# Performance work log

Hardware: AMD Instinct MI355X
Metric: run time of the kernel (lower is better)

## Reference

```python
import jax, jax.numpy as jnp
import numpy as np

SHARED_DIM = 512
ENC_IN = 512
LATENT = 16
BATCH = 65536
NUM_CLASSES = 16


def setup_inputs() -> dict:
    key = jax.random.key(0)
    ks = jax.random.split(key, 12)
    s = 1.0 / np.sqrt(SHARED_DIM)
    si = 1.0 / np.sqrt(ENC_IN)
    return {
        "x": jax.random.normal(ks[0], (BATCH, ENC_IN), dtype=jnp.float32),
        # shared MLP: two ReLU hiddens + identity output (rlkit Mlp)
        "W0": jax.random.uniform(ks[1], (SHARED_DIM, ENC_IN), jnp.float32, -si, si),
        "b0": jnp.zeros((SHARED_DIM,), jnp.float32),
        "W1": jax.random.uniform(ks[2], (SHARED_DIM, SHARED_DIM), jnp.float32, -s, s),
        "b1": jnp.zeros((SHARED_DIM,), jnp.float32),
        "W2": jax.random.uniform(ks[3], (SHARED_DIM, SHARED_DIM), jnp.float32, -s, s),
        "b2": jnp.zeros((SHARED_DIM,), jnp.float32),
        # class encoder (router)
        "Wc": jax.random.uniform(ks[4], (NUM_CLASSES, SHARED_DIM), jnp.float32, -s, s),
        "bc": jnp.zeros((NUM_CLASSES,), jnp.float32),
        # per-class gaussian experts, stacked: [K, 2*latent, shared_dim]
        "Wg": jax.random.uniform(ks[5], (NUM_CLASSES, 2 * LATENT, SHARED_DIM), jnp.float32, -s, s),
        "bg": jnp.zeros((NUM_CLASSES, 2 * LATENT), jnp.float32),
    }


def reference(x, W0, b0, W1, b1, W2, b2, Wc, bc, Wg, bg):
    # shared encoder: ReLU MLP with identity output layer
    m = jax.nn.relu(x @ W0.T + b0)
    m = jax.nn.relu(m @ W1.T + b1)
    m = m @ W2.T + b2                      # [B, D]
    # router: softmax over classes, then most-likely class per sample
    y_probs = jax.nn.softmax(m @ Wc.T + bc, axis=-1)   # [B, K]
    y = jnp.argmax(y_probs, axis=1)                    # [B]
    # evaluate ALL per-class experts densely (as the original does)
    mu_sigma = jnp.einsum('bd,ked->bke', m, Wg) + bg   # [B, K, 2L]
    mu = mu_sigma[..., :LATENT]                        # Normal mean; sampler='mean'
    # gather the selected class's mean per sample
    z = jnp.take_along_axis(mu, y[:, None, None], axis=1)[:, 0, :]  # [B, L]
    return (z, y)
```

## Files before the change

kernel.cpp:

```cpp
#include <hip/hip_runtime.h>
#include <hip/hip_bf16.h>

typedef __attribute__((ext_vector_type(8))) short short8;
typedef __attribute__((ext_vector_type(16))) float floatx16;
typedef __attribute__((ext_vector_type(4))) float floatx4;

#define AS1 __attribute__((address_space(1)))
#define AS3 __attribute__((address_space(3)))

constexpr int MM = 65536;
constexpr int KK = 512;
constexpr int NN = 512;

#define GM 128
#define GN 128
#define GK 32
#define LDT 40

__device__ __forceinline__ unsigned short bf16_rn(float v) {
  unsigned u = __float_as_uint(v);
  return (unsigned short)((u + 0x7FFFu + ((u >> 16) & 1u)) >> 16);
}
__device__ __forceinline__ float bf16_to_f32(unsigned short h) {
  return __uint_as_float((unsigned)h << 16);
}

__global__ __launch_bounds__(256) void split_kernel(
    const float* __restrict__ src, unsigned short* __restrict__ h,
    unsigned short* __restrict__ l, int n4) {
  int i = blockIdx.x * 256 + threadIdx.x;
  if (i >= n4) return;
  float4 v = ((const float4*)src)[i];
  ushort4 hv, lv;
  hv.x = bf16_rn(v.x); lv.x = bf16_rn(v.x - bf16_to_f32(hv.x));
  hv.y = bf16_rn(v.y); lv.y = bf16_rn(v.y - bf16_to_f32(hv.y));
  hv.z = bf16_rn(v.z); lv.z = bf16_rn(v.z - bf16_to_f32(hv.z));
  hv.w = bf16_rn(v.w); lv.w = bf16_rn(v.w - bf16_to_f32(hv.w));
  ((ushort4*)h)[i] = hv;
  ((ushort4*)l)[i] = lv;
}

template<bool RELU>
__global__ __launch_bounds__(512, 1) void gemm_mfma(
    const unsigned short* __restrict__ Ah, const unsigned short* __restrict__ Al,
    const unsigned short* __restrict__ Wh, const unsigned short* __restrict__ Wl,
    const float* __restrict__ bias,
    unsigned short* __restrict__ Ch, unsigned short* __restrict__ Cl) {
  __shared__ __align__(16) unsigned short smem[65536];
  const int tid = threadIdx.x;
  const int lane = tid & 63;
  const int wid = tid >> 6;
  const int wr = wid >> 2;
  const int wc = wid & 3;
  const int nwg = gridDim.x;
  const int hw  = blockIdx.x;
  const int logical = (hw & 7) * (nwg >> 3) + (hw >> 3);
  const int bm = logical >> 1, bn = logical & 1;
  const size_t Abase = (size_t)bm * 256 * KK;
  const size_t Bbase = (size_t)bn * 256 * KK;

  const int sarr  = wid >> 1;
  const int rbase = (wid & 1) * 128;
  const unsigned short* gsrc = (sarr == 0) ? Ah : (sarr == 1) ? Al
                             : (sarr == 2) ? Wh : Wl;
  const size_t tb = (sarr < 2) ? Abase : Bbase;
  const int rowl = lane >> 2;
  const int gch  = (lane & 3) ^ ((lane >> 3) & 3);
  const unsigned short* gbase = gsrc + tb + (size_t)(rbase + rowl) * KK + gch * 8;
  unsigned short* ldst = smem + sarr * 8192 + rbase * 32;

  auto stage2 = [&](int buf, int kk, int p) {
#pragma unroll
    for (int j = p * 2; j < p * 2 + 2; ++j) {
      __builtin_amdgcn_global_load_lds(
          (const AS1 unsigned int*)(gbase + (size_t)(j * 16) * KK + kk),
          (AS3 unsigned int*)(ldst + buf * 32768 + j * 16 * 32),
          16, 0, 0);
    }
  };

  floatx16 acc[4][2];
#pragma unroll
  for (int i = 0; i < 4; ++i)
#pragma unroll
    for (int j = 0; j < 2; ++j)
#pragma unroll
      for (int r = 0; r < 16; ++r) acc[i][j][r] = 0.f;

#pragma unroll
  for (int p = 0; p < 4; ++p) stage2(0, 0, p);

  const int swz = (lane >> 1) & 3;
#pragma unroll
  for (int t = 0; t < 16; ++t) {
    const int cur = t & 1;
    const unsigned short* base = smem + cur * 32768;
    short8 fbh[2], fbl[2];
#pragma unroll
    for (int p = 0; p < 4; ++p) {
      const int ks = p >> 1, h = p & 1;
      const int ch = ks * 2 + (lane >> 5);
      const int sw = (ch ^ swz) * 8;
      short8 fah[2], fal[2];

      if (p == 0) {
        if (t < 15) {
          stage2(cur ^ 1, (t + 1) * GK, 0);
          asm volatile("s_waitcnt vmcnt(2)" ::: "memory");
        } else {
          asm volatile("s_waitcnt vmcnt(0)" ::: "memory");
        }
        __builtin_amdgcn_s_barrier();
        __builtin_amdgcn_sched_barrier(0);
      }

#pragma unroll
      for (int q = 0; q < 2; ++q) {
        int row = wr * 128 + (h * 2 + q) * 32 + (lane & 31);
        fah[q] = *(const short8*)(base + row * 32 + sw);
        fal[q] = *(const short8*)(base + 8192 + row * 32 + sw);
      }
      if (h == 0) {
#pragma unroll
        for (int si = 0; si < 2; ++si) {
          int col = wc * 64 + si * 32 + (lane & 31);
          fbh[si] = *(const short8*)(base + 16384 + col * 32 + sw);
          fbl[si] = *(const short8*)(base + 24576 + col * 32 + sw);
        }
      }

      if (p > 0) {
        if (t < 15) stage2(cur ^ 1, (t + 1) * GK, p);
        __builtin_amdgcn_sched_barrier(0);
        __builtin_amdgcn_s_barrier();
        __builtin_amdgcn_sched_barrier(0);
      }

      __builtin_amdgcn_s_setprio(1);
#pragma unroll
      for (int q = 0; q < 2; ++q)
#pragma unroll
        for (int si = 0; si < 2; ++si) {
          const int ri = h * 2 + q;
          acc[ri][si] = __builtin_amdgcn_mfma_f32_32x32x16_bf16(fah[q], fbh[si], acc[ri][si], 0, 0, 0);
          acc[ri][si] = __builtin_amdgcn_mfma_f32_32x32x16_bf16(fah[q], fbl[si], acc[ri][si], 0, 0, 0);
          acc[ri][si] = __builtin_amdgcn_mfma_f32_32x32x16_bf16(fal[q], fbh[si], acc[ri][si], 0, 0, 0);
        }
      __builtin_amdgcn_s_setprio(0);
      __builtin_amdgcn_sched_barrier(0);
      __builtin_amdgcn_s_barrier();
    }
  }

  float bv[2];
#pragma unroll
  for (int si = 0; si < 2; ++si)
    bv[si] = bias[bn * 256 + wc * 64 + si * 32 + (lane & 31)];

  unsigned* lds32 = (unsigned*)smem;
#pragma unroll
  for (int ri = 0; ri < 4; ++ri) {
    __syncthreads();
#pragma unroll
    for (int si = 0; si < 2; ++si) {
      int lcol = wc * 64 + si * 32 + (lane & 31);
#pragma unroll
      for (int r = 0; r < 16; ++r) {
        int frow = (r & 3) + 8 * (r >> 2) + 4 * (lane >> 5);
        float v = acc[ri][si][r] + bv[si];
        if (RELU) v = fmaxf(v, 0.f);
        unsigned short h = bf16_rn(v);
        unsigned short lo = bf16_rn(v - bf16_to_f32(h));
        lds32[(wr * 32 + frow) * 256 + lcol] = (unsigned)h | ((unsigned)lo << 16);
      }
    }
    __syncthreads();
#pragma unroll
    for (int p = 0; p < 8; ++p) {
      int c = tid + p * 512;
      int lrow = c >> 6;
      int cc = (c & 63) * 4;
      uint4 d = *(const uint4*)&lds32[lrow * 256 + cc];
      ushort4 hv, lv;
      hv.x = (unsigned short)(d.x); lv.x = (unsigned short)(d.x >> 16);
      hv.y = (unsigned short)(d.y); lv.y = (unsigned short)(d.y >> 16);
      hv.z = (unsigned short)(d.z); lv.z = (unsigned short)(d.z >> 16);
      hv.w = (unsigned short)(d.w); lv.w = (unsigned short)(d.w >> 16);
      int grow = bm * 256 + (lrow >> 5) * 128 + ri * 32 + (lrow & 31);
      size_t gi = (size_t)grow * NN + bn * 256 + cc;
      *(ushort4*)&Ch[gi] = hv;
      *(ushort4*)&Cl[gi] = lv;
    }
  }
}

__global__ __launch_bounds__(256, 2) void gemm_muz(
    const unsigned short* __restrict__ Ahm, const unsigned short* __restrict__ Wh,
    const float* __restrict__ bias, const float* __restrict__ y_in,
    float* __restrict__ z_out) {
  __shared__ __align__(16) unsigned short smem[16384];
  unsigned short* sA = smem;
  unsigned short* sB = smem + 8192;
  const int tid = threadIdx.x;
  const int lane = tid & 63;
  const int wid = tid >> 6;
  const int wr = wid >> 1;
  const int wc = wid & 1;
  const int nwg = gridDim.x;
  const int hw  = blockIdx.x;
  const int logical = (hw & 7) * (nwg >> 3) + (hw >> 3);
  const int bm = logical >> 1, bn = logical & 1;
  const size_t Abase = (size_t)bm * GM * KK;
  const size_t Bbase = (size_t)bn * GN * KK;

  const unsigned short* gsrc = (wid < 2) ? Ahm : Wh;
  const size_t tb = (wid < 2) ? Abase : Bbase;
  unsigned short* ldst = (wid < 2) ? sA : sB;
  const int rbase = (wid & 1) * 64;
  const int rowl = lane >> 2;
  const int gch  = (lane & 3) ^ ((lane >> 3) & 3);
  const unsigned short* gbase = gsrc + tb + (size_t)rowl * KK + gch * 8;

  auto stage = [&](int buf, int kk) {
#pragma unroll
    for (int j = 0; j < 4; ++j) {
      const int r0 = rbase + j * 16;
      __builtin_amdgcn_global_load_lds(
          (const AS1 unsigned int*)(gbase + (size_t)r0 * KK + kk),
          (AS3 unsigned int*)(ldst + buf * 4096 + r0 * GK),
          16, 0, 0);
    }
  };

  floatx16 acc[2][2];
#pragma unroll
  for (int i = 0; i < 2; ++i)
#pragma unroll
    for (int j = 0; j < 2; ++j)
#pragma unroll
      for (int r = 0; r < 16; ++r) acc[i][j][r] = 0.f;

  stage(0, 0);

  const int swz = (lane >> 1) & 3;
  int cur = 0;
#pragma unroll
  for (int k0 = 0; k0 < KK; k0 += GK) {
    if (k0 + GK < KK) {
      stage(cur ^ 1, k0 + GK);
      asm volatile("s_waitcnt vmcnt(4)" ::: "memory");
    } else {
      asm volatile("s_waitcnt vmcnt(0)" ::: "memory");
    }
    __builtin_amdgcn_s_barrier();
    __builtin_amdgcn_sched_barrier(0);

    const unsigned short* pA = sA + cur * 4096;
    const unsigned short* pB = sB + cur * 4096;
#pragma unroll
    for (int ks = 0; ks < 2; ++ks) {
      const int ch = ks * 2 + (lane >> 5);
      const int sw = (ch ^ swz) * 8;
      short8 fa[2], fb[2];
#pragma unroll
      for (int ri = 0; ri < 2; ++ri) {
        int row = wr * 64 + ri * 32 + (lane & 31);
        fa[ri] = *(const short8*)(pA + row * GK + sw);
      }
#pragma unroll
      for (int si = 0; si < 2; ++si) {
        int col = wc * 64 + si * 32 + (lane & 31);
        fb[si] = *(const short8*)(pB + col * GK + sw);
      }
#pragma unroll
      for (int ri = 0; ri < 2; ++ri)
#pragma unroll
        for (int si = 0; si < 2; ++si)
          acc[ri][si] = __builtin_amdgcn_mfma_f32_32x32x16_bf16(fa[ri], fb[si], acc[ri][si], 0, 0, 0);
    }
    __builtin_amdgcn_sched_barrier(0);
    __builtin_amdgcn_s_barrier();
    cur ^= 1;
  }

  int colv[2]; float bv[2];
#pragma unroll
  for (int si = 0; si < 2; ++si) {
    colv[si] = bn * GN + wc * 64 + si * 32 + (lane & 31);
    bv[si] = bias[colv[si]];
  }
#pragma unroll
  for (int ri = 0; ri < 2; ++ri)
#pragma unroll
    for (int r = 0; r < 16; ++r) {
      int row = bm * GM + wr * 64 + ri * 32 + (r & 3) + 8 * (r >> 2) + 4 * (lane >> 5);
      int yv = (int)y_in[row];
#pragma unroll
      for (int si = 0; si < 2; ++si) {
        if ((colv[si] >> 4) == yv)
          z_out[(size_t)row * 16 + (colv[si] & 15)] = acc[ri][si][r] + bv[si];
      }
    }
}

__global__ __launch_bounds__(256) void logits_kernel(
    const unsigned short* __restrict__ mh, const unsigned short* __restrict__ ml,
    const unsigned short* __restrict__ wch, const unsigned short* __restrict__ wcl,
    const float* __restrict__ bc, float* __restrict__ y_out) {
  __shared__ unsigned short smh[64][LDT], sml[64][LDT];
  __shared__ float slog[64][17];
  const int tid = threadIdx.x;
  const int lane = tid & 63;
  const int wid = tid >> 6;
  const size_t row0 = (size_t)blockIdx.x * 64;
  const int fr = lane & 15;
  const int fq = lane >> 4;

  floatx4 acc = {0.f, 0.f, 0.f, 0.f};
  const unsigned short* bh = wch + fr * 512 + fq * 8;
  const unsigned short* bl = wcl + fr * 512 + fq * 8;

  for (int k0 = 0; k0 < 512; k0 += 32) {
    {
      int row = tid >> 2, cc = (tid & 3) * 8;
      size_t g = (row0 + row) * 512 + k0 + cc;
      *(short8*)&smh[row][cc] = *(const short8*)(mh + g);
      *(short8*)&sml[row][cc] = *(const short8*)(ml + g);
    }
    __syncthreads();
    short8 ah = *(const short8*)&smh[wid * 16 + fr][fq * 8];
    short8 al = *(const short8*)&sml[wid * 16 + fr][fq * 8];
    short8 fbh = *(const short8*)(bh + k0);
    short8 fbl = *(const short8*)(bl + k0);
    acc = __builtin_amdgcn_mfma_f32_16x16x32_bf16(ah, fbh, acc, 0, 0, 0);
    acc = __builtin_amdgcn_mfma_f32_16x16x32_bf16(ah, fbl, acc, 0, 0, 0);
    acc = __builtin_amdgcn_mfma_f32_16x16x32_bf16(al, fbh, acc, 0, 0, 0);
    __syncthreads();
  }
#pragma unroll
  for (int r = 0; r < 4; ++r)
    slog[wid * 16 + fq * 4 + r][fr] = acc[r] + bc[fr];
  __syncthreads();
  if (tid < 64) {
    float best = slog[tid][0];
    int bi = 0;
#pragma unroll
    for (int j = 1; j < 16; ++j) {
      float v = slog[tid][j];
      if (v > best) { best = v; bi = j; }
    }
    y_out[row0 + tid] = (float)bi;
  }
}

__global__ __launch_bounds__(256) void prep_wg(
    const float* __restrict__ Wg, const float* __restrict__ bg,
    unsigned short* __restrict__ wgh, float* __restrict__ wgb) {
  int gid = blockIdx.x * 256 + threadIdx.x;
  if (gid >= 32768) return;
  int r = gid >> 7;
  int c4 = (gid & 127) * 4;
  int k = r >> 4, e = r & 15;
  float4 v = *(const float4*)(Wg + ((size_t)k * 32 + e) * 512 + c4);
  ushort4 h;
  h.x = bf16_rn(v.x); h.y = bf16_rn(v.y); h.z = bf16_rn(v.z); h.w = bf16_rn(v.w);
  *(ushort4*)(wgh + (size_t)r * 512 + c4) = h;
  if (c4 == 0) wgb[r] = bg[k * 32 + e];
}

extern "C" void kernel_launch(void* const* d_in, const int* in_sizes, int n_in,
                              void* d_out, int out_size, void* d_ws, size_t ws_size,
                              hipStream_t stream) {
  const float* x  = (const float*)d_in[0];
  const float* W0 = (const float*)d_in[1];
  const float* b0 = (const float*)d_in[2];
  const float* W1 = (const float*)d_in[3];
  const float* b1 = (const float*)d_in[4];
  const float* W2 = (const float*)d_in[5];
  const float* b2 = (const float*)d_in[6];
  const float* Wc = (const float*)d_in[7];
  const float* bc = (const float*)d_in[8];
  const float* Wg = (const float*)d_in[9];
  const float* bg = (const float*)d_in[10];

  const size_t NEL = (size_t)MM * KK;
  unsigned short* Ah = (unsigned short*)d_ws;
  unsigned short* Al = Ah + NEL;
  unsigned short* Bh = Al + NEL;
  unsigned short* Bl = Bh + NEL;
  unsigned short* wch = Al;
  unsigned short* wcl = Al + 8192;
  unsigned short* wgh = Al + 16384;
  float* wgb = (float*)(Al + 16384 + 131072);

  unsigned short* w0h = (unsigned short*)d_out;
  unsigned short* w0l = w0h + 262144;
  unsigned short* w1h = w0l + 262144;
  unsigned short* w1l = w1h + 262144;
  unsigned short* w2h = w1l + 262144;
  unsigned short* w2l = w2h + 262144;

  float* z_out = (float*)d_out;
  float* y_out = z_out + (size_t)MM * 16;

  split_kernel<<<(int)(NEL / 4 / 256), 256, 0, stream>>>(x, Ah, Al, (int)(NEL / 4));
  split_kernel<<<256, 256, 0, stream>>>(W0, w0h, w0l, 65536);
  split_kernel<<<256, 256, 0, stream>>>(W1, w1h, w1l, 65536);
  split_kernel<<<256, 256, 0, stream>>>(W2, w2h, w2l, 65536);

  const int ngrid = (MM / 256) * (NN / 256);
  gemm_mfma<true ><<<ngrid, 512, 0, stream>>>(Ah, Al, w0h, w0l, b0, Bh, Bl);
  gemm_mfma<true ><<<ngrid, 512, 0, stream>>>(Bh, Bl, w1h, w1l, b1, Ah, Al);
  gemm_mfma<false><<<ngrid, 512, 0, stream>>>(Ah, Al, w2h, w2l, b2, Bh, Bl);

  split_kernel<<<8, 256, 0, stream>>>(Wc, wch, wcl, 2048);
  prep_wg<<<128, 256, 0, stream>>>(Wg, bg, wgh, wgb);

  logits_kernel<<<MM / 64, 256, 0, stream>>>(Bh, Bl, wch, wcl, bc, y_out);
  gemm_muz<<<(MM / GM) * 2, 256, 0, stream>>>(Bh, wgh, wgb, y_out, z_out);
}
```

Measured before the change: 615.5 us.

## Fuse fp32-to-bf16 split of x into first GEMM and enlarge mu/z GEMM tiles

Drops the standalone split kernel for x. The first layer GEMM now loads fp32 x directly and splits it into hi/lo bf16 in registers before writing to LDS, which removes one full read and write of the 128MB input plus its split arrays. The mu/z GEMM is also restructured to 256x256 tiles with 512 threads, covering all 256 expert columns per block, with finer-grained staging interleaved with MFMA. The cost is more register pressure and in-kernel conversion ALU work in the first GEMM, and a register-prefetched A path instead of direct global-to-LDS loads.

```diff
diff --git a/kernel.cpp b/kernel.cpp
--- a/kernel.cpp
+++ b/kernel.cpp
@@ -12,8 +12,6 @@
 constexpr int KK = 512;
 constexpr int NN = 512;
 
-#define GM 128
-#define GN 128
 #define GK 32
 #define LDT 40
 
@@ -194,106 +192,289 @@
   }
 }
 
-__global__ __launch_bounds__(256, 2) void gemm_muz(
-    const unsigned short* __restrict__ Ahm, const unsigned short* __restrict__ Wh,
-    const float* __restrict__ bias, const float* __restrict__ y_in,
-    float* __restrict__ z_out) {
-  __shared__ __align__(16) unsigned short smem[16384];
-  unsigned short* sA = smem;
-  unsigned short* sB = smem + 8192;
+__global__ __launch_bounds__(512, 1) void gemm_x(
+    const float* __restrict__ X,
+    const unsigned short* __restrict__ Wh, const unsigned short* __restrict__ Wl,
+    const float* __restrict__ bias,
+    unsigned short* __restrict__ Ch, unsigned short* __restrict__ Cl) {
+  __shared__ __align__(16) unsigned short smem[65536];
   const int tid = threadIdx.x;
   const int lane = tid & 63;
   const int wid = tid >> 6;
-  const int wr = wid >> 1;
-  const int wc = wid & 1;
+  const int wr = wid >> 2;
+  const int wc = wid & 3;
   const int nwg = gridDim.x;
   const int hw  = blockIdx.x;
   const int logical = (hw & 7) * (nwg >> 3) + (hw >> 3);
   const int bm = logical >> 1, bn = logical & 1;
-  const size_t Abase = (size_t)bm * GM * KK;
-  const size_t Bbase = (size_t)bn * GN * KK;
-
-  const unsigned short* gsrc = (wid < 2) ? Ahm : Wh;
-  const size_t tb = (wid < 2) ? Abase : Bbase;
-  unsigned short* ldst = (wid < 2) ? sA : sB;
-  const int rbase = (wid & 1) * 64;
+
+  const int barr = wid >> 2;
+  const int brb  = (wid & 3) * 64;
   const int rowl = lane >> 2;
   const int gch  = (lane & 3) ^ ((lane >> 3) & 3);
-  const unsigned short* gbase = gsrc + tb + (size_t)rowl * KK + gch * 8;
-
-  auto stage = [&](int buf, int kk) {
+  const unsigned short* gbB = (barr ? Wl : Wh) + (size_t)bn * 256 * KK
+                            + (size_t)(brb + rowl) * KK + gch * 8;
+  unsigned short* ldB = smem + (2 + barr) * 8192 + brb * 32;
+
+  auto stageB = [&](int buf, int kk) {
 #pragma unroll
     for (int j = 0; j < 4; ++j) {
-      const int r0 = rbase + j * 16;
       __builtin_amdgcn_global_load_lds(
-          (const AS1 unsigned int*)(gbase + (size_t)r0 * KK + kk),
-          (AS3 unsigned int*)(ldst + buf * 4096 + r0 * GK),
+          (const AS1 unsigned int*)(gbB + (size_t)(j * 16) * KK + kk),
+          (AS3 unsigned int*)(ldB + buf * 32768 + j * 16 * 32),
           16, 0, 0);
     }
   };
 
-  floatx16 acc[2][2];
-#pragma unroll
-  for (int i = 0; i < 2; ++i)
+  const int arow = lane >> 3;
+  const int akc  = lane & 7;
+  const float* gx = X + ((size_t)(bm * 256 + wid * 32) + arow) * KK + akc * 4;
+  auto loadA = [&](int kk, float4* av) {
+#pragma unroll
+    for (int j = 0; j < 4; ++j)
+      av[j] = *(const float4*)(gx + (size_t)(j * 8) * KK + kk);
+  };
+  const int apc = ((akc >> 1) ^ ((arow >> 1) & 3));
+  const int aoff = (wid * 32 + arow) * 32 + apc * 8 + (akc & 1) * 4;
+  auto writeA = [&](int buf, const float4* av) {
+#pragma unroll
+    for (int j = 0; j < 4; ++j) {
+      ushort4 hv, lv;
+      hv.x = bf16_rn(av[j].x); lv.x = bf16_rn(av[j].x - bf16_to_f32(hv.x));
+      hv.y = bf16_rn(av[j].y); lv.y = bf16_rn(av[j].y - bf16_to_f32(hv.y));
+      hv.z = bf16_rn(av[j].z); lv.z = bf16_rn(av[j].z - bf16_to_f32(hv.z));
+      hv.w = bf16_rn(av[j].w); lv.w = bf16_rn(av[j].w - bf16_to_f32(hv.w));
+      int o = buf * 32768 + aoff + j * 8 * 32;
+      *(ushort4*)(smem + o) = hv;
+      *(ushort4*)(smem + 8192 + o) = lv;
+    }
+  };
+
+  floatx16 acc[4][2];
+#pragma unroll
+  for (int i = 0; i < 4; ++i)
 #pragma unroll
     for (int j = 0; j < 2; ++j)
 #pragma unroll
       for (int r = 0; r < 16; ++r) acc[i][j][r] = 0.f;
 
-  stage(0, 0);
+  {
+    float4 av0[4];
+    stageB(0, 0);
+    loadA(0, av0);
+    asm volatile("s_waitcnt vmcnt(0)" ::: "memory");
+    writeA(0, av0);
+    asm volatile("s_waitcnt lgkmcnt(0)" ::: "memory");
+    __builtin_amdgcn_s_barrier();
+  }
 
   const int swz = (lane >> 1) & 3;
-  int cur = 0;
-#pragma unroll
-  for (int k0 = 0; k0 < KK; k0 += GK) {
-    if (k0 + GK < KK) {
-      stage(cur ^ 1, k0 + GK);
-      asm volatile("s_waitcnt vmcnt(4)" ::: "memory");
-    } else {
-      asm volatile("s_waitcnt vmcnt(0)" ::: "memory");
-    }
-    __builtin_amdgcn_s_barrier();
-    __builtin_amdgcn_sched_barrier(0);
-
-    const unsigned short* pA = sA + cur * 4096;
-    const unsigned short* pB = sB + cur * 4096;
-#pragma unroll
-    for (int ks = 0; ks < 2; ++ks) {
+#pragma unroll
+  for (int t = 0; t < 16; ++t) {
+    const int cur = t & 1;
+    const unsigned short* base = smem + cur * 32768;
+    short8 fbh[2], fbl[2];
+    float4 av[4];
+#pragma unroll
+    for (int p = 0; p < 4; ++p) {
+      const int ks = p >> 1, h = p & 1;
       const int ch = ks * 2 + (lane >> 5);
       const int sw = (ch ^ swz) * 8;
-      short8 fa[2], fb[2];
-#pragma unroll
-      for (int ri = 0; ri < 2; ++ri) {
-        int row = wr * 64 + ri * 32 + (lane & 31);
-        fa[ri] = *(const short8*)(pA + row * GK + sw);
-      }
-#pragma unroll
-      for (int si = 0; si < 2; ++si) {
-        int col = wc * 64 + si * 32 + (lane & 31);
-        fb[si] = *(const short8*)(pB + col * GK + sw);
-      }
-#pragma unroll
-      for (int ri = 0; ri < 2; ++ri)
+      short8 fah[2], fal[2];
+
+      if (p == 0 && t < 15) {
+        stageB(cur ^ 1, (t + 1) * GK);
+        loadA((t + 1) * GK, av);
+      }
+
+#pragma unroll
+      for (int q = 0; q < 2; ++q) {
+        int row = wr * 128 + (h * 2 + q) * 32 + (lane & 31);
+        fah[q] = *(const short8*)(base + row * 32 + sw);
+        fal[q] = *(const short8*)(base + 8192 + row * 32 + sw);
+      }
+      if (h == 0) {
+#pragma unroll
+        for (int si = 0; si < 2; ++si) {
+          int col = wc * 64 + si * 32 + (lane & 31);
+          fbh[si] = *(const short8*)(base + 16384 + col * 32 + sw);
+          fbl[si] = *(const short8*)(base + 24576 + col * 32 + sw);
+        }
+      }
+
+      __builtin_amdgcn_s_setprio(1);
+#pragma unroll
+      for (int q = 0; q < 2; ++q)
+#pragma unroll
+        for (int si = 0; si < 2; ++si) {
+          const int ri = h * 2 + q;
+          acc[ri][si] = __builtin_amdgcn_mfma_f32_32x32x16_bf16(fah[q], fbh[si], acc[ri][si], 0, 0, 0);
+          acc[ri][si] = __builtin_amdgcn_mfma_f32_32x32x16_bf16(fah[q], fbl[si], acc[ri][si], 0, 0, 0);
+          acc[ri][si] = __builtin_amdgcn_mfma_f32_32x32x16_bf16(fal[q], fbh[si], acc[ri][si], 0, 0, 0);
+        }
+      __builtin_amdgcn_s_setprio(0);
+      __builtin_amdgcn_sched_barrier(0);
+
+      if (p == 3) {
+        if (t < 15) {
+          asm volatile("s_waitcnt vmcnt(0)" ::: "memory");
+          writeA(cur ^ 1, av);
+        }
+        asm volatile("s_waitcnt lgkmcnt(0)" ::: "memory");
+        __builtin_amdgcn_s_barrier();
+      } else {
+        __builtin_amdgcn_s_barrier();
+      }
+      __builtin_amdgcn_sched_barrier(0);
+    }
+  }
+
+  float bv[2];
+#pragma unroll
+  for (int si = 0; si < 2; ++si)
+    bv[si] = bias[bn * 256 + wc * 64 + si * 32 + (lane & 31)];
+
+  unsigned* lds32 = (unsigned*)smem;
+#pragma unroll
+  for (int ri = 0; ri < 4; ++ri) {
+    __syncthreads();
+#pragma unroll
+    for (int si = 0; si < 2; ++si) {
+      int lcol = wc * 64 + si * 32 + (lane & 31);
+#pragma unroll
+      for (int r = 0; r < 16; ++r) {
+        int frow = (r & 3) + 8 * (r >> 2) + 4 * (lane >> 5);
+        float v = fmaxf(acc[ri][si][r] + bv[si], 0.f);
+        unsigned short h = bf16_rn(v);
+        unsigned short lo = bf16_rn(v - bf16_to_f32(h));
+        lds32[(wr * 32 + frow) * 256 + lcol] = (unsigned)h | ((unsigned)lo << 16);
+      }
+    }
+    __syncthreads();
+#pragma unroll
+    for (int p = 0; p < 8; ++p) {
+      int c = tid + p * 512;
+      int lrow = c >> 6;
+      int cc = (c & 63) * 4;
+      uint4 d = *(const uint4*)&lds32[lrow * 256 + cc];
+      ushort4 hv, lv;
+      hv.x = (unsigned short)(d.x); lv.x = (unsigned short)(d.x >> 16);
+      hv.y = (unsigned short)(d.y); lv.y = (unsigned short)(d.y >> 16);
+      hv.z = (unsigned short)(d.z); lv.z = (unsigned short)(d.z >> 16);
+      hv.w = (unsigned short)(d.w); lv.w = (unsigned short)(d.w >> 16);
+      int grow = bm * 256 + (lrow >> 5) * 128 + ri * 32 + (lrow & 31);
+      size_t gi = (size_t)grow * NN + bn * 256 + cc;
+      *(ushort4*)&Ch[gi] = hv;
+      *(ushort4*)&Cl[gi] = lv;
+    }
+  }
+}
+
+__global__ __launch_bounds__(512) void gemm_muz(
+    const unsigned short* __restrict__ Ahm, const unsigned short* __restrict__ Wh,
+    const float* __restrict__ bias, const float* __restrict__ y_in,
+    float* __restrict__ z_out) {
+  __shared__ __align__(16) unsigned short smem[32768];
+  const int tid = threadIdx.x;
+  const int lane = tid & 63;
+  const int wid = tid >> 6;
+  const int wr = wid >> 2;
+  const int wc = wid & 3;
+  const int bm = blockIdx.x;
+
+  const int sarr = (wid < 4) ? 0 : 1;
+  const int rb   = (wid & 3) * 64;
+  const unsigned short* gsrc = sarr ? Wh : (Ahm + (size_t)bm * 256 * KK);
+  const int rowl = lane >> 2;
+  const int gch  = (lane & 3) ^ ((lane >> 3) & 3);
+  const unsigned short* gbase = gsrc + (size_t)(rb + rowl) * KK + gch * 8;
+  unsigned short* ldst = smem + sarr * 8192 + rb * 32;
+
+  auto stage1 = [&](int buf, int kk, int j) {
+    __builtin_amdgcn_global_load_lds(
+        (const AS1 unsigned int*)(gbase + (size_t)(j * 16) * KK + kk),
+        (AS3 unsigned int*)(ldst + buf * 16384 + j * 16 * 32),
+        16, 0, 0);
+  };
+
+  floatx16 acc[4][2];
+#pragma unroll
+  for (int i = 0; i < 4; ++i)
+#pragma unroll
+    for (int j = 0; j < 2; ++j)
+#pragma unroll
+      for (int r = 0; r < 16; ++r) acc[i][j][r] = 0.f;
+
+#pragma unroll
+  for (int j = 0; j < 4; ++j) stage1(0, 0, j);
+
+  const int swz = (lane >> 1) & 3;
+#pragma unroll
+  for (int t = 0; t < 16; ++t) {
+    const int cur = t & 1;
+    const unsigned short* base = smem + cur * 16384;
+    short8 fb[2];
+#pragma unroll
+    for (int p = 0; p < 4; ++p) {
+      const int ks = p >> 1, h = p & 1;
+      const int ch = ks * 2 + (lane >> 5);
+      const int sw = (ch ^ swz) * 8;
+      short8 fa[2];
+
+      if (p == 0) {
+        if (t < 15) {
+          stage1(cur ^ 1, (t + 1) * GK, 0);
+          asm volatile("s_waitcnt vmcnt(1)" ::: "memory");
+        } else {
+          asm volatile("s_waitcnt vmcnt(0)" ::: "memory");
+        }
+        __builtin_amdgcn_s_barrier();
+        __builtin_amdgcn_sched_barrier(0);
+      }
+
+#pragma unroll
+      for (int q = 0; q < 2; ++q) {
+        int row = wr * 128 + (h * 2 + q) * 32 + (lane & 31);
+        fa[q] = *(const short8*)(base + row * 32 + sw);
+      }
+      if (h == 0) {
+#pragma unroll
+        for (int si = 0; si < 2; ++si) {
+          int col = wc * 64 + si * 32 + (lane & 31);
+          fb[si] = *(const short8*)(base + 8192 + col * 32 + sw);
+        }
+      }
+
+      if (p > 0) {
+        if (t < 15) stage1(cur ^ 1, (t + 1) * GK, p);
+        __builtin_amdgcn_sched_barrier(0);
+        __builtin_amdgcn_s_barrier();
+        __builtin_amdgcn_sched_barrier(0);
+      }
+
+      __builtin_amdgcn_s_setprio(1);
+#pragma unroll
+      for (int q = 0; q < 2; ++q)
 #pragma unroll
         for (int si = 0; si < 2; ++si)
-          acc[ri][si] = __builtin_amdgcn_mfma_f32_32x32x16_bf16(fa[ri], fb[si], acc[ri][si], 0, 0, 0);
-    }
-    __builtin_amdgcn_sched_barrier(0);
-    __builtin_amdgcn_s_barrier();
-    cur ^= 1;
+          acc[h * 2 + q][si] = __builtin_amdgcn_mfma_f32_32x32x16_bf16(fa[q], fb[si], acc[h * 2 + q][si], 0, 0, 0);
+      __builtin_amdgcn_s_setprio(0);
+      __builtin_amdgcn_sched_barrier(0);
+      __builtin_amdgcn_s_barrier();
+    }
   }
 
   int colv[2]; float bv[2];
 #pragma unroll
   for (int si = 0; si < 2; ++si) {
-    colv[si] = bn * GN + wc * 64 + si * 32 + (lane & 31);
+    colv[si] = wc * 64 + si * 32 + (lane & 31);
     bv[si] = bias[colv[si]];
   }
 #pragma unroll
-  for (int ri = 0; ri < 2; ++ri)
+  for (int ri = 0; ri < 4; ++ri)
 #pragma unroll
     for (int r = 0; r < 16; ++r) {
-      int row = bm * GM + wr * 64 + ri * 32 + (r & 3) + 8 * (r >> 2) + 4 * (lane >> 5);
+      int row = bm * 256 + wr * 128 + ri * 32 + (r & 3) + 8 * (r >> 2) + 4 * (lane >> 5);
       int yv = (int)y_in[row];
 #pragma unroll
       for (int si = 0; si < 2; ++si) {
@@ -403,13 +584,12 @@
   float* z_out = (float*)d_out;
   float* y_out = z_out + (size_t)MM * 16;
 
-  split_kernel<<<(int)(NEL / 4 / 256), 256, 0, stream>>>(x, Ah, Al, (int)(NEL / 4));
   split_kernel<<<256, 256, 0, stream>>>(W0, w0h, w0l, 65536);
   split_kernel<<<256, 256, 0, stream>>>(W1, w1h, w1l, 65536);
   split_kernel<<<256, 256, 0, stream>>>(W2, w2h, w2l, 65536);
 
   const int ngrid = (MM / 256) * (NN / 256);
-  gemm_mfma<true ><<<ngrid, 512, 0, stream>>>(Ah, Al, w0h, w0l, b0, Bh, Bl);
+  gemm_x<<<ngrid, 512, 0, stream>>>(x, w0h, w0l, b0, Bh, Bl);
   gemm_mfma<true ><<<ngrid, 512, 0, stream>>>(Bh, Bl, w1h, w1l, b1, Ah, Al);
   gemm_mfma<false><<<ngrid, 512, 0, stream>>>(Ah, Al, w2h, w2l, b2, Bh, Bl);
 
@@ -417,5 +597,5 @@
   prep_wg<<<128, 256, 0, stream>>>(Wg, bg, wgh, wgb);
 
   logits_kernel<<<MM / 64, 256, 0, stream>>>(Bh, Bl, wch, wcl, bc, y_out);
-  gemm_muz<<<(MM / GM) * 2, 256, 0, stream>>>(Bh, wgh, wgb, y_out, z_out);
-}
+  gemm_muz<<<MM / 256, 512, 0, stream>>>(Bh, wgh, wgb, y_out, z_out);
+}
```

Result: faster. 587.0 us (-4.6%).
